# Kernel tuning notes

Measured on AMD Instinct MI355X. Metric: run time of the kernel, lower is better.

Reference implementation:

```python
import jax, jax.numpy as jnp
import numpy as np

NUM_ITEMS = 50000
EMBED_DIM = 100
HIDDEN_DIM = 200
BATCH = 1024
SEQ_LEN = 200


def setup_inputs() -> dict:
    key = jax.random.key(0)
    ks = jax.random.split(key, 8)
    q = jax.random.randint(ks[0], (BATCH, SEQ_LEN), 0, NUM_ITEMS, dtype=jnp.int32)
    embed = jax.random.normal(ks[1], (NUM_ITEMS, EMBED_DIM), jnp.float32) * 0.05
    # GRU weights, concatenated along gate axis in order (r, z, n)
    Wi = jax.random.normal(ks[2], (EMBED_DIM, 3 * HIDDEN_DIM), jnp.float32) * (1.0 / np.sqrt(EMBED_DIM))
    bi = jnp.zeros((3 * HIDDEN_DIM,), jnp.float32)  # input-side biases (flax dense_i has bias)
    Wh = jax.random.normal(ks[3], (HIDDEN_DIM, 3 * HIDDEN_DIM), jnp.float32) * (1.0 / np.sqrt(HIDDEN_DIM))
    bhn = jnp.zeros((HIDDEN_DIM,), jnp.float32)  # only the 'hn' hidden dense has a bias in flax GRUCell
    Wo = jax.random.normal(ks[4], (HIDDEN_DIM, NUM_ITEMS), jnp.float32) * (1.0 / np.sqrt(HIDDEN_DIM))
    bo = jnp.zeros((NUM_ITEMS,), jnp.float32)
    return {"q": q, "embed": embed, "Wi": Wi, "bi": bi, "Wh": Wh, "bhn": bhn, "Wo": Wo, "bo": bo}


def reference(q, embed, Wi, bi, Wh, bhn, Wo, bo):
    # mask padding id 0, then embed
    not_zero = (q != 0).astype(jnp.float32)[..., None]        # [B,T,1]
    x = jnp.take(embed, q, axis=0) * not_zero                 # [B,T,E]
    H = Wh.shape[0]

    def step(h, xt):
        gi = xt @ Wi + bi                                     # [B,3H]
        gh = h @ Wh                                           # [B,3H]
        ir, iz, inn = jnp.split(gi, 3, axis=-1)
        hr, hz, hn = jnp.split(gh, 3, axis=-1)
        r = jax.nn.sigmoid(ir + hr)
        z = jax.nn.sigmoid(iz + hz)
        n = jnp.tanh(inn + r * (hn + bhn))
        h_new = (1.0 - z) * n + z * h                          # flax GRUCell update
        return h_new, None

    h0 = jnp.zeros((q.shape[0], H), jnp.float32)
    xT = jnp.swapaxes(x, 0, 1)                                # [T,B,E]
    h_last, _ = jax.lax.scan(step, h0, xT)
    return h_last @ Wo + bo                                    # [B, num_items]
```

## Files before the change

kernel.cpp:

```cpp
#include <hip/hip_runtime.h>

#define BATCH 1024
#define TT    200
#define EE    100
#define HH    200
#define GG    600
#define NI    50000
#define NKT   7
#define KPAD  224
#define HSTR  264
#define NTILE3 3125
#define NTW   50
#define KTW   4

typedef _Float16 half8 __attribute__((ext_vector_type(8)));
typedef _Float16 half4v __attribute__((ext_vector_type(4)));
typedef float   float4v __attribute__((ext_vector_type(4)));

static __device__ __forceinline__ float4v mfma16(half8 a, half8 b, float4v c) {
    return __builtin_amdgcn_mfma_f32_16x16x32_f16(a, b, c, 0, 0, 0);
}

#if __has_builtin(__builtin_amdgcn_rcpf)
static __device__ __forceinline__ float fastrcp(float x) { return __builtin_amdgcn_rcpf(x); }
#else
static __device__ __forceinline__ float fastrcp(float x) { return 1.f / x; }
#endif

static __device__ __forceinline__ float sigm(float x) {
    return fastrcp(1.f + __expf(-x));
}
static __device__ __forceinline__ float tanh_fast(float x) {
    float e = __expf(2.f * fabsf(x));
    float t = 1.f - 2.f * fastrcp(e + 1.f);
    return __builtin_copysignf(t, x);
}

__global__ __launch_bounds__(64) void repack_all(const float* __restrict__ Wi,
                                                 const float* __restrict__ bi,
                                                 const float* __restrict__ Wh,
                                                 half8* __restrict__ Wif,
                                                 float* __restrict__ biP,
                                                 half8* __restrict__ Whf) {
    const int bx   = blockIdx.x;
    const int lane = threadIdx.x;
    const int l15  = lane & 15;
    const int lhi  = lane >> 4;
    if (bx < NTW * KTW) {
        const int kt = bx & 3;
        const int nt = bx >> 2;
        const int np = nt * 16 + l15;
        const int c  = np >> 2;
        const int g  = np & 3;
        half8 v;
        #pragma unroll
        for (int j = 0; j < 8; ++j) {
            int k = kt * 32 + lhi * 8 + j;
            float w = (k < EE && g < 3) ? Wi[(size_t)k * GG + g * HH + c] : 0.f;
            v[j] = (_Float16)w;
        }
        Wif[(size_t)bx * 64 + lane] = v;
        if (kt == 0 && lhi == 0)
            biP[np] = (g < 3) ? bi[g * HH + c] : 0.f;
    } else {
        const int b2   = bx - NTW * KTW;
        const int kt   = b2 % NKT;
        const int tile = b2 / NKT;
        const int g    = tile / 16;
        const int tc   = tile % 16;
        const int col  = tc * 16 + l15;
        half8 v;
        #pragma unroll
        for (int j = 0; j < 8; ++j) {
            int k = kt * 32 + lhi * 8 + j;
            float w = (k < HH && col < HH) ? Wh[(size_t)k * GG + g * HH + col] : 0.f;
            v[j] = (_Float16)w;
        }
        Whf[(size_t)b2 * 64 + lane] = v;
    }
}

__global__ __launch_bounds__(256) void ewi_mfma(const float* __restrict__ embed,
                                                const half8* __restrict__ Wif,
                                                const float* __restrict__ biP,
                                                _Float16* __restrict__ EWi16) {
    const int tid  = threadIdx.x;
    const int w    = tid >> 6;
    const int lane = tid & 63;
    const int l15  = lane & 15;
    const int lhi  = lane >> 4;

    const int mtb   = (blockIdx.x * 4 + w) * 2;
    const bool liveA = (mtb < NTILE3);
    const bool liveB = (mtb + 1 < NTILE3);
    if (!liveA) return;
    const int i0a = mtb * 16;
    const int i0b = liveB ? (mtb + 1) * 16 : i0a;

    half8 aA[KTW], aB[KTW];
    #pragma unroll
    for (int kt = 0; kt < KTW; ++kt) {
        const int k0 = kt * 32 + lhi * 8;
        const float* erA = embed + (size_t)(i0a + l15) * EE + k0;
        const float* erB = embed + (size_t)(i0b + l15) * EE + k0;
        #pragma unroll
        for (int j = 0; j < 8; ++j) {
            aA[kt][j] = (k0 + j < EE) ? (_Float16)erA[j] : (_Float16)0.f;
            aB[kt][j] = (k0 + j < EE) ? (_Float16)erB[j] : (_Float16)0.f;
        }
    }

    for (int nt = 0; nt < NTW; ++nt) {
        const half8* bfp = Wif + (size_t)nt * KTW * 64 + lane;
        float4v accA = (float4v){0.f, 0.f, 0.f, 0.f};
        float4v accB = (float4v){0.f, 0.f, 0.f, 0.f};
        #pragma unroll
        for (int kt = 0; kt < KTW; ++kt) {
            const half8 bf = bfp[kt * 64];
            accA = mfma16(aA[kt], bf, accA);
            accB = mfma16(aB[kt], bf, accB);
        }
        const float biv = biP[nt * 16 + l15];
        #pragma unroll
        for (int r = 0; r < 4; ++r) {
            const int rowA = i0a + lhi * 4 + r;
            float valA = accA[r] + biv;
            if (rowA == 0) valA = biv;
            EWi16[(size_t)rowA * 800 + nt * 16 + l15] = (_Float16)valA;
        }
        if (liveB) {
            #pragma unroll
            for (int r = 0; r < 4; ++r) {
                const int rowB = i0b + lhi * 4 + r;
                EWi16[(size_t)rowB * 800 + nt * 16 + l15] = (_Float16)(accB[r] + biv);
            }
        }
    }
}

__global__ __launch_bounds__(512, 2) void scan_mfma(const int* __restrict__ q,
                                                    const _Float16* __restrict__ EWi16,
                                                    const half8* __restrict__ Whf,
                                                    const float* __restrict__ bhn,
                                                    _Float16* __restrict__ h16g) {
    __shared__ __align__(16) _Float16 hbuf[2][16 * HSTR];
    __shared__ __align__(16) float accbuf[16 * 49 * 4];
    __shared__ int qs[4][TT];

    const int tid  = threadIdx.x;
    const int w    = tid >> 6;
    const int lane = tid & 63;
    const int l15  = lane & 15;
    const int lhi  = lane >> 4;
    const int b0   = blockIdx.x * 4;

    for (int idx = tid; idx < 2 * 16 * HSTR; idx += 512)
        ((_Float16*)hbuf)[idx] = (_Float16)0.f;
    for (int idx = tid; idx < 4 * TT; idx += 512) {
        int b = idx / TT, t = idx % TT;
        qs[b][t] = q[(size_t)(b0 + b) * TT + t];
    }

    half8 wb[3][2][7];
    #pragma unroll
    for (int g = 0; g < 3; ++g) {
        #pragma unroll
        for (int c2 = 0; c2 < 2; ++c2) {
            const int tc = w + c2 * 8;
            #pragma unroll
            for (int kt = 0; kt < NKT; ++kt)
                wb[g][c2][kt] = Whf[((size_t)(g * 16 + tc) * NKT + kt) * 64 + lane];
        }
    }

    const int col0 = w * 16 + l15;
    const int col1 = 128 + w * 16 + l15;
    const bool v1  = (col1 < HH);
    const int colw1 = v1 ? col1 : 236;
    const float bh0 = bhn[col0];
    const float bh1 = v1 ? bhn[col1] : 0.f;

    float hreg0 = 0.f, hreg1 = 0.f;

    __syncthreads();

    half4v giA0, giA1, giB0, giB1;
    #define LOADGI(d0, d1, tt) do {                                          \
        const int qv = qs[lhi][tt];                                          \
        const _Float16* ew = EWi16 + (size_t)qv * 800;                       \
        d0 = *(const half4v*)(ew + col0 * 4);                                \
        d1 = *(const half4v*)(ew + col1 * 4);                                \
    } while (0)

    LOADGI(giA0, giA1, 0);
    LOADGI(giB0, giB1, 1);

    #define STEP(CUR, NXT, G0, G1, TLOAD) do {                               \
        float4v acc[3][2];                                                   \
        _Pragma("unroll")                                                    \
        for (int g = 0; g < 3; ++g)                                          \
            _Pragma("unroll")                                                \
            for (int c2 = 0; c2 < 2; ++c2)                                   \
                acc[g][c2] = (float4v){0.f, 0.f, 0.f, 0.f};                  \
        const _Float16* hb = &hbuf[CUR][0];                                  \
        _Pragma("unroll")                                                    \
        for (int kt = 0; kt < NKT; ++kt) {                                   \
            const half8 af = *(const half8*)(hb + l15 * HSTR + kt * 32 + lhi * 8); \
            _Pragma("unroll")                                                \
            for (int g = 0; g < 3; ++g) {                                    \
                acc[g][0] = mfma16(af, wb[g][0][kt], acc[g][0]);             \
                acc[g][1] = mfma16(af, wb[g][1][kt], acc[g][1]);             \
            }                                                                \
        }                                                                    \
                \
        if (lane < 16) {                                                     \
            _Pragma("unroll")                                                \
            for (int g = 0; g < 3; ++g)                                      \
                _Pragma("unroll")                                            \
                for (int c2 = 0; c2 < 2; ++c2)                               \
                    *(float4v*)&accbuf[((l15 * 49) + (g * 16 + w + c2 * 8)) * 4] = acc[g][c2]; \
        }                                                                    \
                              \
        _Float16* hn = &hbuf[NXT][0];                                        \
        {                                                                    \
            const int rowb = l15 * 49 * 4 + lhi;                             \
            float aR0 = accbuf[rowb + (0 * 16 + w) * 4];                     \
            float aZ0 = accbuf[rowb + (1 * 16 + w) * 4];                     \
            float aN0 = accbuf[rowb + (2 * 16 + w) * 4];                     \
            float aR1 = accbuf[rowb + (0 * 16 + w + 8) * 4];                 \
            float aZ1 = accbuf[rowb + (1 * 16 + w + 8) * 4];                 \
            float aN1 = accbuf[rowb + (2 * 16 + w + 8) * 4];                 \
            float r0 = sigm((float)G0[0] + aR0);                             \
            float z0 = sigm((float)G0[1] + aZ0);                             \
            float n0 = tanh_fast((float)G0[2] + r0 * (aN0 + bh0));           \
            float hv0 = (1.f - z0) * n0 + z0 * hreg0;                        \
            hreg0 = hv0;                                                     \
            hn[lhi * HSTR + col0] = (_Float16)hv0;                           \
            float r1 = sigm((float)G1[0] + aR1);                             \
            float z1 = sigm((float)G1[1] + aZ1);                             \
            float n1 = tanh_fast((float)G1[2] + r1 * (aN1 + bh1));           \
            float hv1 = (1.f - z1) * n1 + z1 * hreg1;                        \
            hreg1 = hv1;                                                     \
            hn[lhi * HSTR + colw1] = (_Float16)hv1;                          \
        }                                                                    \
         \
        {                                                                    \
            const int tl = (TLOAD) < TT ? (TLOAD) : (TT - 1);                \
            LOADGI(G0, G1, tl);                                              \
        }                                                                    \
        __syncthreads();                                                     \
    } while (0)

    for (int t = 0; t < TT; t += 2) {
        STEP(0, 1, giA0, giA1, t + 2);
        STEP(1, 0, giB0, giB1, t + 3);
    }
    #undef STEP
    #undef LOADGI

    for (int idx = tid; idx < 4 * KPAD; idx += 512) {
        int b = idx / KPAD, k = idx % KPAD;
        h16g[(size_t)(b0 + b) * KPAD + k] = hbuf[0][b * HSTR + k];
    }
}

__global__ __launch_bounds__(256) void out_mfma(const _Float16* __restrict__ h16g,
                                                const float* __restrict__ Wo,
                                                const float* __restrict__ bo,
                                                float* __restrict__ out) {
    const int tid  = threadIdx.x;
    const int w    = tid >> 6;
    const int lane = tid & 63;
    const int l15  = lane & 15;
    const int lhi  = lane >> 4;

    const int ntb   = (blockIdx.x * 4 + w) * 2;
    const bool liveA = (ntb < NTILE3);
    const bool liveB = (ntb + 1 < NTILE3);
    const int ntA = liveA ? ntb : (NTILE3 - 1);
    const int ntB = liveB ? (ntb + 1) : (NTILE3 - 1);
    const int colA = ntA * 16 + l15;
    const int colB = ntB * 16 + l15;

    half8 wbA[7], wbB[7];
    #pragma unroll
    for (int kt = 0; kt < NKT; ++kt) {
        #pragma unroll
        for (int j = 0; j < 8; ++j) {
            int k = kt * 32 + lhi * 8 + j;
            wbA[kt][j] = (k < HH) ? (_Float16)Wo[(size_t)k * NI + colA] : (_Float16)0.f;
            wbB[kt][j] = (k < HH) ? (_Float16)Wo[(size_t)k * NI + colB] : (_Float16)0.f;
        }
    }
    const float bovA = bo[colA];
    const float bovB = bo[colB];

    for (int mt = 0; mt < BATCH / 16; ++mt) {
        const _Float16* hrow = h16g + (size_t)(mt * 16 + l15) * KPAD + lhi * 8;
        float4v accA = (float4v){0.f, 0.f, 0.f, 0.f};
        float4v accB = (float4v){0.f, 0.f, 0.f, 0.f};
        #pragma unroll
        for (int kt = 0; kt < NKT; ++kt) {
            const half8 af = *(const half8*)(hrow + kt * 32);
            accA = mfma16(af, wbA[kt], accA);
            accB = mfma16(af, wbB[kt], accB);
        }
        if (liveA) {
            #pragma unroll
            for (int r = 0; r < 4; ++r) {
                int row = mt * 16 + lhi * 4 + r;
                out[(size_t)row * NI + colA] = accA[r] + bovA;
            }
        }
        if (liveB) {
            #pragma unroll
            for (int r = 0; r < 4; ++r) {
                int row = mt * 16 + lhi * 4 + r;
                out[(size_t)row * NI + colB] = accB[r] + bovB;
            }
        }
    }
}

extern "C" void kernel_launch(void* const* d_in, const int* in_sizes, int n_in,
                              void* d_out, int out_size, void* d_ws, size_t ws_size,
                              hipStream_t stream) {
    const int*   q     = (const int*)d_in[0];
    const float* embed = (const float*)d_in[1];
    const float* Wi    = (const float*)d_in[2];
    const float* bi    = (const float*)d_in[3];
    const float* Wh    = (const float*)d_in[4];
    const float* bhn   = (const float*)d_in[5];
    const float* Wo    = (const float*)d_in[6];
    const float* bo    = (const float*)d_in[7];
    float* out = (float*)d_out;

    _Float16* EWi16 = (_Float16*)d_out;
    half8*    Whf   = (half8*)((char*)d_out + 120000000);
    half8*    Wif   = (half8*)((char*)d_out + 121000000);
    float*    biP   = (float*)((char*)d_out + 122000000);
    _Float16* h16g  = (_Float16*)d_ws;

    repack_all<<<NTW * KTW + 48 * NKT, 64, 0, stream>>>(Wi, bi, Wh, Wif, biP, Whf);
    ewi_mfma<<<(NTILE3 / 2 + 3) / 4, 256, 0, stream>>>(embed, Wif, biP, EWi16);
    scan_mfma<<<BATCH / 4, 512, 0, stream>>>(q, EWi16, Whf, bhn, h16g);
    out_mfma<<<(NTILE3 / 2 + 3) / 4 + 1, 256, 0, stream>>>(h16g, Wo, bo, out);
}
```

Baseline: 374.9 us.

## Process 16 batch rows per scan block and keep gate accumulators in registers

The GRU scan kernel now handles 16 sequences per block instead of 4, so each MFMA tile row holds a real batch element rather than padding. The MFMA operands are swapped so the output layout puts hidden columns in lane groups. That lets each lane apply the gate nonlinearities straight from its accumulators, removing the LDS accumulator round trip. The cost is only 64 blocks on the GPU, which lowers parallelism, so per-step latency now dominates the scan.

```diff
diff --git a/kernel.cpp b/kernel.cpp
--- a/kernel.cpp
+++ b/kernel.cpp
@@ -144,24 +144,23 @@
                                                     const float* __restrict__ bhn,
                                                     _Float16* __restrict__ h16g) {
     __shared__ __align__(16) _Float16 hbuf[2][16 * HSTR];
-    __shared__ __align__(16) float accbuf[16 * 49 * 4];
-    __shared__ int qs[4][TT];
+    __shared__ int qs[TT][16];
 
     const int tid  = threadIdx.x;
     const int w    = tid >> 6;
     const int lane = tid & 63;
     const int l15  = lane & 15;
     const int lhi  = lane >> 4;
-    const int b0   = blockIdx.x * 4;
+    const int b0   = blockIdx.x * 16;
 
     for (int idx = tid; idx < 2 * 16 * HSTR; idx += 512)
         ((_Float16*)hbuf)[idx] = (_Float16)0.f;
-    for (int idx = tid; idx < 4 * TT; idx += 512) {
-        int b = idx / TT, t = idx % TT;
-        qs[b][t] = q[(size_t)(b0 + b) * TT + t];
-    }
-
-    half8 wb[3][2][7];
+    for (int idx = tid; idx < 16 * TT; idx += 512) {
+        int b = idx & 15, t = idx >> 4;
+        qs[t][b] = q[(size_t)(b0 + b) * TT + t];
+    }
+
+    half8 wa[3][2][7];
     #pragma unroll
     for (int g = 0; g < 3; ++g) {
         #pragma unroll
@@ -169,96 +168,104 @@
             const int tc = w + c2 * 8;
             #pragma unroll
             for (int kt = 0; kt < NKT; ++kt)
-                wb[g][c2][kt] = Whf[((size_t)(g * 16 + tc) * NKT + kt) * 64 + lane];
-        }
-    }
-
-    const int col0 = w * 16 + l15;
-    const int col1 = 128 + w * 16 + l15;
-    const bool v1  = (col1 < HH);
-    const int colw1 = v1 ? col1 : 236;
-    const float bh0 = bhn[col0];
-    const float bh1 = v1 ? bhn[col1] : 0.f;
-
-    float hreg0 = 0.f, hreg1 = 0.f;
+                wa[g][c2][kt] = Whf[((size_t)(g * 16 + tc) * NKT + kt) * 64 + lane];
+        }
+    }
+
+    const int cb0  = w * 16 + lhi * 4;
+    const int cb1  = (w + 8) * 16 + lhi * 4;
+    const bool pad1 = (cb1 >= HH);
+    const int gb1  = pad1 ? 0 : cb1;
+
+    float bh0[4], bh1[4];
+    #pragma unroll
+    for (int r = 0; r < 4; ++r) {
+        bh0[r] = bhn[cb0 + r];
+        int c1 = cb1 + r; bh1[r] = bhn[c1 < HH ? c1 : 0];
+    }
+
+    float hr0[4] = {0.f, 0.f, 0.f, 0.f};
+    float hr1[4] = {0.f, 0.f, 0.f, 0.f};
 
     __syncthreads();
 
-    half4v giA0, giA1, giB0, giB1;
-    #define LOADGI(d0, d1, tt) do {                                          \
-        const int qv = qs[lhi][tt];                                          \
+    half8 g0a, g0b, g1a, g1b;
+    #define LOADGI(tt) do {                                                  \
+        const int tl = (tt) < TT ? (tt) : (TT - 1);                          \
+        const int qv = qs[tl][l15];                                          \
         const _Float16* ew = EWi16 + (size_t)qv * 800;                       \
-        d0 = *(const half4v*)(ew + col0 * 4);                                \
-        d1 = *(const half4v*)(ew + col1 * 4);                                \
+        g0a = *(const half8*)(ew + cb0 * 4);                                 \
+        g0b = *(const half8*)(ew + cb0 * 4 + 8);                             \
+        g1a = *(const half8*)(ew + gb1 * 4);                                 \
+        g1b = *(const half8*)(ew + gb1 * 4 + 8);                             \
     } while (0)
 
-    LOADGI(giA0, giA1, 0);
-    LOADGI(giB0, giB1, 1);
-
-    #define STEP(CUR, NXT, G0, G1, TLOAD) do {                               \
-        float4v acc[3][2];                                                   \
+    LOADGI(0);
+
+    #define COMBINE_HALF(ga, gb, aR, aZ, aN, bh, hr, cbase, isPad) do {      \
+        half4v hv4;                                                          \
         _Pragma("unroll")                                                    \
-        for (int g = 0; g < 3; ++g)                                          \
+        for (int r = 0; r < 4; ++r) {                                        \
+            float gr, gz, gn;                                                \
+            if      (r == 0) { gr = (float)ga[0]; gz = (float)ga[1]; gn = (float)ga[2]; } \
+            else if (r == 1) { gr = (float)ga[4]; gz = (float)ga[5]; gn = (float)ga[6]; } \
+            else if (r == 2) { gr = (float)gb[0]; gz = (float)gb[1]; gn = (float)gb[2]; } \
+            else             { gr = (float)gb[4]; gz = (float)gb[5]; gn = (float)gb[6]; } \
+            float rr = sigm(gr + aR[r]);                                     \
+            float zz = sigm(gz + aZ[r]);                                     \
+            float nn = tanh_fast(gn + rr * (aN[r] + bh[r]));                 \
+            float hv = (1.f - zz) * nn + zz * hr[r];                         \
+            if (isPad) hv = 0.f;           \
+            hr[r] = hv;                                                      \
+            hv4[r] = (_Float16)hv;                                           \
+        }                                                                    \
+        *(half4v*)(hn + l15 * HSTR + (cbase)) = hv4;                         \
+    } while (0)
+
+    #define STEP(CUR, NXT, TLOAD) do {                                       \
+        const _Float16* hb = &hbuf[CUR][0];                                  \
+        _Float16*       hn = &hbuf[NXT][0];                                  \
+        half8 bf[NKT];                                                       \
+        _Pragma("unroll")                                                    \
+        for (int kt = 0; kt < NKT; ++kt)                                     \
+            bf[kt] = *(const half8*)(hb + l15 * HSTR + kt * 32 + lhi * 8);   \
+        {                                                                    \
+            float4v aR = (float4v){0.f,0.f,0.f,0.f};                         \
+            float4v aZ = (float4v){0.f,0.f,0.f,0.f};                         \
+            float4v aN = (float4v){0.f,0.f,0.f,0.f};                         \
             _Pragma("unroll")                                                \
-            for (int c2 = 0; c2 < 2; ++c2)                                   \
-                acc[g][c2] = (float4v){0.f, 0.f, 0.f, 0.f};                  \
-        const _Float16* hb = &hbuf[CUR][0];                                  \
-        _Pragma("unroll")                                                    \
-        for (int kt = 0; kt < NKT; ++kt) {                                   \
-            const half8 af = *(const half8*)(hb + l15 * HSTR + kt * 32 + lhi * 8); \
+            for (int kt = 0; kt < NKT; ++kt) {                               \
+                aR = mfma16(wa[0][0][kt], bf[kt], aR);                       \
+                aZ = mfma16(wa[1][0][kt], bf[kt], aZ);                       \
+                aN = mfma16(wa[2][0][kt], bf[kt], aN);                       \
+            }                                                                \
+            COMBINE_HALF(g0a, g0b, aR, aZ, aN, bh0, hr0, cb0, false);        \
+        }                                                                    \
+        {                                                                    \
+            float4v aR = (float4v){0.f,0.f,0.f,0.f};                         \
+            float4v aZ = (float4v){0.f,0.f,0.f,0.f};                         \
+            float4v aN = (float4v){0.f,0.f,0.f,0.f};                         \
             _Pragma("unroll")                                                \
-            for (int g = 0; g < 3; ++g) {                                    \
-                acc[g][0] = mfma16(af, wb[g][0][kt], acc[g][0]);             \
-                acc[g][1] = mfma16(af, wb[g][1][kt], acc[g][1]);             \
+            for (int kt = 0; kt < NKT; ++kt) {                               \
+                aR = mfma16(wa[0][1][kt], bf[kt], aR);                       \
+                aZ = mfma16(wa[1][1][kt], bf[kt], aZ);                       \
+                aN = mfma16(wa[2][1][kt], bf[kt], aN);                       \
             }                                                                \
+            COMBINE_HALF(g1a, g1b, aR, aZ, aN, bh1, hr1, cb1, pad1);         \
         }                                                                    \
-                \
-        if (lane < 16) {                                                     \
-            _Pragma("unroll")                                                \
-            for (int g = 0; g < 3; ++g)                                      \
-                _Pragma("unroll")                                            \
-                for (int c2 = 0; c2 < 2; ++c2)                               \
-                    *(float4v*)&accbuf[((l15 * 49) + (g * 16 + w + c2 * 8)) * 4] = acc[g][c2]; \
-        }                                                                    \
-                              \
-        _Float16* hn = &hbuf[NXT][0];                                        \
-        {                                                                    \
-            const int rowb = l15 * 49 * 4 + lhi;                             \
-            float aR0 = accbuf[rowb + (0 * 16 + w) * 4];                     \
-            float aZ0 = accbuf[rowb + (1 * 16 + w) * 4];                     \
-            float aN0 = accbuf[rowb + (2 * 16 + w) * 4];                     \
-            float aR1 = accbuf[rowb + (0 * 16 + w + 8) * 4];                 \
-            float aZ1 = accbuf[rowb + (1 * 16 + w + 8) * 4];                 \
-            float aN1 = accbuf[rowb + (2 * 16 + w + 8) * 4];                 \
-            float r0 = sigm((float)G0[0] + aR0);                             \
-            float z0 = sigm((float)G0[1] + aZ0);                             \
-            float n0 = tanh_fast((float)G0[2] + r0 * (aN0 + bh0));           \
-            float hv0 = (1.f - z0) * n0 + z0 * hreg0;                        \
-            hreg0 = hv0;                                                     \
-            hn[lhi * HSTR + col0] = (_Float16)hv0;                           \
-            float r1 = sigm((float)G1[0] + aR1);                             \
-            float z1 = sigm((float)G1[1] + aZ1);                             \
-            float n1 = tanh_fast((float)G1[2] + r1 * (aN1 + bh1));           \
-            float hv1 = (1.f - z1) * n1 + z1 * hreg1;                        \
-            hreg1 = hv1;                                                     \
-            hn[lhi * HSTR + colw1] = (_Float16)hv1;                          \
-        }                                                                    \
-         \
-        {                                                                    \
-            const int tl = (TLOAD) < TT ? (TLOAD) : (TT - 1);                \
-            LOADGI(G0, G1, tl);                                              \
-        }                                                                    \
+        LOADGI(TLOAD);      \
         __syncthreads();                                                     \
     } while (0)
 
     for (int t = 0; t < TT; t += 2) {
-        STEP(0, 1, giA0, giA1, t + 2);
-        STEP(1, 0, giB0, giB1, t + 3);
+        STEP(0, 1, t + 1);
+        STEP(1, 0, t + 2);
     }
     #undef STEP
+    #undef COMBINE_HALF
     #undef LOADGI
 
-    for (int idx = tid; idx < 4 * KPAD; idx += 512) {
+    for (int idx = tid; idx < 16 * KPAD; idx += 512) {
         int b = idx / KPAD, k = idx % KPAD;
         h16g[(size_t)(b0 + b) * KPAD + k] = hbuf[0][b * HSTR + k];
     }
@@ -343,6 +350,6 @@
 
     repack_all<<<NTW * KTW + 48 * NKT, 64, 0, stream>>>(Wi, bi, Wh, Wif, biP, Whf);
     ewi_mfma<<<(NTILE3 / 2 + 3) / 4, 256, 0, stream>>>(embed, Wif, biP, EWi16);
-    scan_mfma<<<BATCH / 4, 512, 0, stream>>>(q, EWi16, Whf, bhn, h16g);
+    scan_mfma<<<BATCH / 16, 512, 0, stream>>>(q, EWi16, Whf, bhn, h16g);
     out_mfma<<<(NTILE3 / 2 + 3) / 4 + 1, 256, 0, stream>>>(h16g, Wo, bo, out);
 }
```

Result: slower. 454.0 us (+21.1%).

## Shrink GRU scan block to four waves and skip padded gate tiles

Applied to the files above, without the earlier changes.

The recurrent scan kernel now runs 256 threads (4 waves) per block instead of 512. Each wave handles up to 10 of the 39 real 16-column gate tiles, where the old layout computed 48 tiles including padding. Gate accumulators are exchanged through a reorganised LDS buffer, with an added barrier between the MFMA store and the gate nonlinearity. Each wave now issues more MFMAs and holds more weight registers, which can lengthen the per-step critical path in exchange for fewer redundant tiles and lower per-block thread overhead.

```diff
diff --git a/kernel.cpp b/kernel.cpp
--- a/kernel.cpp
+++ b/kernel.cpp
@@ -138,13 +138,13 @@
     }
 }
 
-__global__ __launch_bounds__(512, 2) void scan_mfma(const int* __restrict__ q,
+__global__ __launch_bounds__(256, 1) void scan_mfma(const int* __restrict__ q,
                                                     const _Float16* __restrict__ EWi16,
                                                     const half8* __restrict__ Whf,
                                                     const float* __restrict__ bhn,
                                                     _Float16* __restrict__ h16g) {
     __shared__ __align__(16) _Float16 hbuf[2][16 * HSTR];
-    __shared__ __align__(16) float accbuf[16 * 49 * 4];
+    __shared__ __align__(16) float accbuf[39 * 64];
     __shared__ int qs[4][TT];
 
     const int tid  = threadIdx.x;
@@ -154,111 +154,107 @@
     const int lhi  = lane >> 4;
     const int b0   = blockIdx.x * 4;
 
-    for (int idx = tid; idx < 2 * 16 * HSTR; idx += 512)
+    for (int idx = tid; idx < 2 * 16 * HSTR; idx += 256)
         ((_Float16*)hbuf)[idx] = (_Float16)0.f;
-    for (int idx = tid; idx < 4 * TT; idx += 512) {
+    for (int idx = tid; idx < 4 * TT; idx += 256) {
         int b = idx / TT, t = idx % TT;
         qs[b][t] = q[(size_t)(b0 + b) * TT + t];
     }
 
-    half8 wb[3][2][7];
+    half8 wb[10][NKT];
     #pragma unroll
-    for (int g = 0; g < 3; ++g) {
-        #pragma unroll
-        for (int c2 = 0; c2 < 2; ++c2) {
-            const int tc = w + c2 * 8;
-            #pragma unroll
-            for (int kt = 0; kt < NKT; ++kt)
-                wb[g][c2][kt] = Whf[((size_t)(g * 16 + tc) * NKT + kt) * 64 + lane];
-        }
-    }
-
-    const int col0 = w * 16 + l15;
-    const int col1 = 128 + w * 16 + l15;
-    const bool v1  = (col1 < HH);
-    const int colw1 = v1 ? col1 : 236;
-    const float bh0 = bhn[col0];
-    const float bh1 = v1 ? bhn[col1] : 0.f;
-
-    float hreg0 = 0.f, hreg1 = 0.f;
+    for (int i = 0; i < 10; ++i) {
+        int tau = w + 4 * i;
+        if (tau > 38) tau = 38;
+        const int g  = (tau >= 26) ? 2 : (tau >= 13 ? 1 : 0);
+        const int tc = tau - g * 13;
+        #pragma unroll
+        for (int kt = 0; kt < NKT; ++kt)
+            wb[i][kt] = Whf[((size_t)(g * 16 + tc) * NKT + kt) * 64 + lane];
+    }
+    const bool has9 = (w < 3);
+
+    const int cb = lane & 3;
+    const int cc = (lane >> 2) & 15;
+    float bhn_s[4]; bool creal[4]; int cga[4];
+    #pragma unroll
+    for (int j = 0; j < 4; ++j) {
+        const int tc = j * 4 + w;
+        const int cg = tc * 16 + cc;
+        creal[j] = (tc < 13) && (cg < HH);
+        cga[j]   = cg;
+        bhn_s[j] = creal[j] ? bhn[cg] : 0.f;
+    }
+    float hreg[4] = {0.f, 0.f, 0.f, 0.f};
 
     __syncthreads();
 
-    half4v giA0, giA1, giB0, giB1;
-    #define LOADGI(d0, d1, tt) do {                                          \
-        const int qv = qs[lhi][tt];                                          \
+    half4v gA[4], gB[4];
+    #define LOADGI(G, tt) do {                                               \
+        const int tl = (tt) < TT ? (tt) : (TT - 1);                          \
+        const int qv = qs[cb][tl];                                           \
         const _Float16* ew = EWi16 + (size_t)qv * 800;                       \
-        d0 = *(const half4v*)(ew + col0 * 4);                                \
-        d1 = *(const half4v*)(ew + col1 * 4);                                \
+        G[0] = *(const half4v*)(ew + (size_t)(w * 16 + cc) * 4);             \
+        G[1] = *(const half4v*)(ew + (size_t)((4 + w) * 16 + cc) * 4);       \
+        G[2] = *(const half4v*)(ew + (size_t)((8 + w) * 16 + cc) * 4);       \
+        if (w == 0 && creal[3])                                              \
+            G[3] = *(const half4v*)(ew + (size_t)(192 + cc) * 4);            \
     } while (0)
 
-    LOADGI(giA0, giA1, 0);
-    LOADGI(giB0, giB1, 1);
-
-    #define STEP(CUR, NXT, G0, G1, TLOAD) do {                               \
-        float4v acc[3][2];                                                   \
+    LOADGI(gA, 0);
+    LOADGI(gB, 1);
+
+    #define STEP(CUR, NXT, G, TLOAD) do {                                    \
+        const _Float16* hb = &hbuf[CUR][0];                                  \
+        float4v acc[10];                                                     \
         _Pragma("unroll")                                                    \
-        for (int g = 0; g < 3; ++g)                                          \
-            _Pragma("unroll")                                                \
-            for (int c2 = 0; c2 < 2; ++c2)                                   \
-                acc[g][c2] = (float4v){0.f, 0.f, 0.f, 0.f};                  \
-        const _Float16* hb = &hbuf[CUR][0];                                  \
+        for (int i = 0; i < 10; ++i) acc[i] = (float4v){0.f, 0.f, 0.f, 0.f}; \
         _Pragma("unroll")                                                    \
         for (int kt = 0; kt < NKT; ++kt) {                                   \
             const half8 af = *(const half8*)(hb + l15 * HSTR + kt * 32 + lhi * 8); \
             _Pragma("unroll")                                                \
-            for (int g = 0; g < 3; ++g) {                                    \
-                acc[g][0] = mfma16(af, wb[g][0][kt], acc[g][0]);             \
-                acc[g][1] = mfma16(af, wb[g][1][kt], acc[g][1]);             \
+            for (int i = 0; i < 9; ++i)                                      \
+                acc[i] = mfma16(af, wb[i][kt], acc[i]);                      \
+            if (has9) acc[9] = mfma16(af, wb[9][kt], acc[9]);                \
+        }                                                                    \
+                  \
+        if (lane < 16) {                                                     \
+            _Pragma("unroll")                                                \
+            for (int i = 0; i < 9; ++i)                                      \
+                *(float4v*)&accbuf[(w + 4 * i) * 64 + l15 * 4] = acc[i];     \
+            if (has9) *(float4v*)&accbuf[(w + 36) * 64 + l15 * 4] = acc[9];  \
+        }                                                                    \
+        __syncthreads();                      \
+        _Float16* hn = &hbuf[NXT][0];                                        \
+        _Pragma("unroll")                                                    \
+        for (int j = 0; j < 4; ++j) {                                        \
+            const int tc = j * 4 + w;                                        \
+            if (tc < 13) {                                 \
+                const float aR = accbuf[(0 * 13 + tc) * 64 + lane];          \
+                const float aZ = accbuf[(1 * 13 + tc) * 64 + lane];          \
+                const float aN = accbuf[(2 * 13 + tc) * 64 + lane];          \
+                if (creal[j]) {                                              \
+                    float rr = sigm((float)G[j][0] + aR);                    \
+                    float zz = sigm((float)G[j][1] + aZ);                    \
+                    float nn = tanh_fast((float)G[j][2] + rr * (aN + bhn_s[j])); \
+                    float hv = (1.f - zz) * nn + zz * hreg[j];               \
+                    hreg[j] = hv;                                            \
+                    hn[cb * HSTR + cga[j]] = (_Float16)hv;                   \
+                }                                                            \
             }                                                                \
         }                                                                    \
-                \
-        if (lane < 16) {                                                     \
-            _Pragma("unroll")                                                \
-            for (int g = 0; g < 3; ++g)                                      \
-                _Pragma("unroll")                                            \
-                for (int c2 = 0; c2 < 2; ++c2)                               \
-                    *(float4v*)&accbuf[((l15 * 49) + (g * 16 + w + c2 * 8)) * 4] = acc[g][c2]; \
-        }                                                                    \
-                              \
-        _Float16* hn = &hbuf[NXT][0];                                        \
-        {                                                                    \
-            const int rowb = l15 * 49 * 4 + lhi;                             \
-            float aR0 = accbuf[rowb + (0 * 16 + w) * 4];                     \
-            float aZ0 = accbuf[rowb + (1 * 16 + w) * 4];                     \
-            float aN0 = accbuf[rowb + (2 * 16 + w) * 4];                     \
-            float aR1 = accbuf[rowb + (0 * 16 + w + 8) * 4];                 \
-            float aZ1 = accbuf[rowb + (1 * 16 + w + 8) * 4];                 \
-            float aN1 = accbuf[rowb + (2 * 16 + w + 8) * 4];                 \
-            float r0 = sigm((float)G0[0] + aR0);                             \
-            float z0 = sigm((float)G0[1] + aZ0);                             \
-            float n0 = tanh_fast((float)G0[2] + r0 * (aN0 + bh0));           \
-            float hv0 = (1.f - z0) * n0 + z0 * hreg0;                        \
-            hreg0 = hv0;                                                     \
-            hn[lhi * HSTR + col0] = (_Float16)hv0;                           \
-            float r1 = sigm((float)G1[0] + aR1);                             \
-            float z1 = sigm((float)G1[1] + aZ1);                             \
-            float n1 = tanh_fast((float)G1[2] + r1 * (aN1 + bh1));           \
-            float hv1 = (1.f - z1) * n1 + z1 * hreg1;                        \
-            hreg1 = hv1;                                                     \
-            hn[lhi * HSTR + colw1] = (_Float16)hv1;                          \
-        }                                                                    \
-         \
-        {                                                                    \
-            const int tl = (TLOAD) < TT ? (TLOAD) : (TT - 1);                \
-            LOADGI(G0, G1, tl);                                              \
-        }                                                                    \
-        __syncthreads();                                                     \
+        LOADGI(G, TLOAD);     \
+        __syncthreads();                                        \
     } while (0)
 
     for (int t = 0; t < TT; t += 2) {
-        STEP(0, 1, giA0, giA1, t + 2);
-        STEP(1, 0, giB0, giB1, t + 3);
+        STEP(0, 1, gA, t + 2);
+        STEP(1, 0, gB, t + 3);
     }
     #undef STEP
     #undef LOADGI
 
-    for (int idx = tid; idx < 4 * KPAD; idx += 512) {
+    for (int idx = tid; idx < 4 * KPAD; idx += 256) {
         int b = idx / KPAD, k = idx % KPAD;
         h16g[(size_t)(b0 + b) * KPAD + k] = hbuf[0][b * HSTR + k];
     }
@@ -343,6 +339,6 @@
 
     repack_all<<<NTW * KTW + 48 * NKT, 64, 0, stream>>>(Wi, bi, Wh, Wif, biP, Whf);
     ewi_mfma<<<(NTILE3 / 2 + 3) / 4, 256, 0, stream>>>(embed, Wif, biP, EWi16);
-    scan_mfma<<<BATCH / 4, 512, 0, stream>>>(q, EWi16, Whf, bhn, h16g);
+    scan_mfma<<<BATCH / 4, 256, 0, stream>>>(q, EWi16, Whf, bhn, h16g);
     out_mfma<<<(NTILE3 / 2 + 3) / 4 + 1, 256, 0, stream>>>(h16g, Wo, bo, out);
 }
```

Measured after the change: 463.5 us. +23.6%, slower.

## Fold hn bias into Wh padding row and issue next gate loads earlier

Applied to the files above, without the earlier changes.

The hidden-side n-gate bias is now stored as an extra row of the packed Wh (row k=HH), and the hidden state buffer holds a constant 1.0 in that padded column. The MFMA therefore produces hn+bhn directly, which removes the per-step bias add and the bhn register loads. The global load of the next step's input gates is also moved to the start of each step, after saving the current values into floats, so its latency overlaps the matrix multiply. The cost is the bias being rounded to fp16 inside the weights, plus a few more live registers.

```diff
diff --git a/kernel.cpp b/kernel.cpp
--- a/kernel.cpp
+++ b/kernel.cpp
@@ -39,6 +39,7 @@
 __global__ __launch_bounds__(64) void repack_all(const float* __restrict__ Wi,
                                                  const float* __restrict__ bi,
                                                  const float* __restrict__ Wh,
+                                                 const float* __restrict__ bhn,
                                                  half8* __restrict__ Wif,
                                                  float* __restrict__ biP,
                                                  half8* __restrict__ Whf) {
@@ -73,7 +74,11 @@
         #pragma unroll
         for (int j = 0; j < 8; ++j) {
             int k = kt * 32 + lhi * 8 + j;
-            float w = (k < HH && col < HH) ? Wh[(size_t)k * GG + g * HH + col] : 0.f;
+            float w = 0.f;
+            if (col < HH) {
+                if (k < HH)                      w = Wh[(size_t)k * GG + g * HH + col];
+                else if (g == 2 && k == HH)      w = bhn[col];
+            }
             v[j] = (_Float16)w;
         }
         Whf[(size_t)b2 * 64 + lane] = v;
@@ -141,7 +146,6 @@
 __global__ __launch_bounds__(512, 2) void scan_mfma(const int* __restrict__ q,
                                                     const _Float16* __restrict__ EWi16,
                                                     const half8* __restrict__ Whf,
-                                                    const float* __restrict__ bhn,
                                                     _Float16* __restrict__ h16g) {
     __shared__ __align__(16) _Float16 hbuf[2][16 * HSTR];
     __shared__ __align__(16) float accbuf[16 * 49 * 4];
@@ -155,7 +159,7 @@
     const int b0   = blockIdx.x * 4;
 
     for (int idx = tid; idx < 2 * 16 * HSTR; idx += 512)
-        ((_Float16*)hbuf)[idx] = (_Float16)0.f;
+        ((_Float16*)hbuf)[idx] = (idx % HSTR == HH) ? (_Float16)1.0f : (_Float16)0.f;
     for (int idx = tid; idx < 4 * TT; idx += 512) {
         int b = idx / TT, t = idx % TT;
         qs[b][t] = q[(size_t)(b0 + b) * TT + t];
@@ -177,8 +181,6 @@
     const int col1 = 128 + w * 16 + l15;
     const bool v1  = (col1 < HH);
     const int colw1 = v1 ? col1 : 236;
-    const float bh0 = bhn[col0];
-    const float bh1 = v1 ? bhn[col1] : 0.f;
 
     float hreg0 = 0.f, hreg1 = 0.f;
 
@@ -186,7 +188,8 @@
 
     half4v giA0, giA1, giB0, giB1;
     #define LOADGI(d0, d1, tt) do {                                          \
-        const int qv = qs[lhi][tt];                                          \
+        const int tl = (tt) < TT ? (tt) : (TT - 1);                          \
+        const int qv = qs[lhi][tl];                                          \
         const _Float16* ew = EWi16 + (size_t)qv * 800;                       \
         d0 = *(const half4v*)(ew + col0 * 4);                                \
         d1 = *(const half4v*)(ew + col1 * 4);                                \
@@ -196,6 +199,10 @@
     LOADGI(giB0, giB1, 1);
 
     #define STEP(CUR, NXT, G0, G1, TLOAD) do {                               \
+            \
+        const float c0r = (float)G0[0], c0z = (float)G0[1], c0n = (float)G0[2]; \
+        const float c1r = (float)G1[0], c1z = (float)G1[1], c1n = (float)G1[2]; \
+        LOADGI(G0, G1, TLOAD);                                               \
         float4v acc[3][2];                                                   \
         _Pragma("unroll")                                                    \
         for (int g = 0; g < 3; ++g)                                          \
@@ -220,7 +227,7 @@
                 for (int c2 = 0; c2 < 2; ++c2)                               \
                     *(float4v*)&accbuf[((l15 * 49) + (g * 16 + w + c2 * 8)) * 4] = acc[g][c2]; \
         }                                                                    \
-                              \
+           \
         _Float16* hn = &hbuf[NXT][0];                                        \
         {                                                                    \
             const int rowb = l15 * 49 * 4 + lhi;                             \
@@ -230,23 +237,18 @@
             float aR1 = accbuf[rowb + (0 * 16 + w + 8) * 4];                 \
             float aZ1 = accbuf[rowb + (1 * 16 + w + 8) * 4];                 \
             float aN1 = accbuf[rowb + (2 * 16 + w + 8) * 4];                 \
-            float r0 = sigm((float)G0[0] + aR0);                             \
-            float z0 = sigm((float)G0[1] + aZ0);                             \
-            float n0 = tanh_fast((float)G0[2] + r0 * (aN0 + bh0));           \
+            float r0 = sigm(c0r + aR0);                                      \
+            float z0 = sigm(c0z + aZ0);                                      \
+            float n0 = tanh_fast(c0n + r0 * aN0);                            \
             float hv0 = (1.f - z0) * n0 + z0 * hreg0;                        \
             hreg0 = hv0;                                                     \
             hn[lhi * HSTR + col0] = (_Float16)hv0;                           \
-            float r1 = sigm((float)G1[0] + aR1);                             \
-            float z1 = sigm((float)G1[1] + aZ1);                             \
-            float n1 = tanh_fast((float)G1[2] + r1 * (aN1 + bh1));           \
+            float r1 = sigm(c1r + aR1);                                      \
+            float z1 = sigm(c1z + aZ1);                                      \
+            float n1 = tanh_fast(c1n + r1 * aN1);                            \
             float hv1 = (1.f - z1) * n1 + z1 * hreg1;                        \
             hreg1 = hv1;                                                     \
             hn[lhi * HSTR + colw1] = (_Float16)hv1;                          \
-        }                                                                    \
-         \
-        {                                                                    \
-            const int tl = (TLOAD) < TT ? (TLOAD) : (TT - 1);                \
-            LOADGI(G0, G1, tl);                                              \
         }                                                                    \
         __syncthreads();                                                     \
     } while (0)
@@ -341,8 +343,8 @@
     float*    biP   = (float*)((char*)d_out + 122000000);
     _Float16* h16g  = (_Float16*)d_ws;
 
-    repack_all<<<NTW * KTW + 48 * NKT, 64, 0, stream>>>(Wi, bi, Wh, Wif, biP, Whf);
+    repack_all<<<NTW * KTW + 48 * NKT, 64, 0, stream>>>(Wi, bi, Wh, bhn, Wif, biP, Whf);
     ewi_mfma<<<(NTILE3 / 2 + 3) / 4, 256, 0, stream>>>(embed, Wif, biP, EWi16);
-    scan_mfma<<<BATCH / 4, 512, 0, stream>>>(q, EWi16, Whf, bhn, h16g);
+    scan_mfma<<<BATCH / 4, 512, 0, stream>>>(q, EWi16, Whf, h16g);
     out_mfma<<<(NTILE3 / 2 + 3) / 4 + 1, 256, 0, stream>>>(h16g, Wo, bo, out);
 }
```

Result: no change. 373.1 us, median of 2 (-0.5%).
